# Performance work log

Measured on AMD Instinct MI355X. Metric: run time of the kernel, lower is better.

The kernel has to match this reference:

```python
import math
import jax, jax.numpy as jnp
import numpy as np

H = 8
DIM = 256
HD = DIM // H
SCALE = math.sqrt(HD)
EPS = 1e-16


def _segment_softmax(scores, dst, num_nodes):
    # scores: [E, H], dst: [E] -> softmax over edges sharing the same dst
    m = jax.ops.segment_max(scores, dst, num_segments=num_nodes)  # [N, H]
    m = jnp.where(jnp.isfinite(m), m, 0.0)  # empty segments -> -inf -> 0
    e = jnp.exp(scores - m[dst])
    s = jax.ops.segment_sum(e, dst, num_segments=num_nodes)  # [N, H]
    return e / (s[dst] + EPS)


def _graph_attention(x, edges, wq, bq, wk, bk, wv, bv, wo, bo):
    # x: [N, DIM]; edges: [2, E] (src, dst). Dropout is identity (eval mode).
    N = x.shape[0]
    Q = (x @ wq + bq).reshape(N, H, HD)
    K = (x @ wk + bk).reshape(N, H, HD)
    V = (x @ wv + bv).reshape(N, H, HD)
    src, dst = edges[0], edges[1]
    scores = jnp.einsum('ehd,ehd->eh', Q[dst], K[src]) / SCALE  # [E, H]
    attn = _segment_softmax(scores, dst, N)  # [E, H]
    msgs = V[src] * attn[:, :, None]  # [E, H, HD]
    out = jax.ops.segment_sum(msgs, dst, num_segments=N).reshape(N, DIM)
    return out @ wo + bo


def _linear_params(key, fan_in, fan_out):
    k1, k2 = jax.random.split(key)
    bound = 1.0 / math.sqrt(fan_in)
    w = jax.random.uniform(k1, (fan_in, fan_out), minval=-bound, maxval=bound, dtype=jnp.float32)
    b = jax.random.uniform(k2, (fan_out,), minval=-bound, maxval=bound, dtype=jnp.float32)
    return w, b


def setup_inputs() -> dict:
    key = jax.random.key(0)
    ks = jax.random.split(key, 12)
    n_slot, n_dom = 20000, 1000
    e_slot, e_dom = 320000, 16000
    inp = {
        'slot_x': jax.random.normal(ks[0], (n_slot, DIM), dtype=jnp.float32),
        'domain_x': jax.random.normal(ks[1], (n_dom, DIM), dtype=jnp.float32),
        'slot_edges': jax.random.randint(ks[2], (2, e_slot), 0, n_slot, dtype=jnp.int32),
        'domain_edges': jax.random.randint(ks[3], (2, e_dom), 0, n_dom, dtype=jnp.int32),
    }
    names = ['wq', 'wk', 'wv', 'wo']
    for i, nm in enumerate(names):
        w, b = _linear_params(ks[4 + i], DIM, DIM)
        inp[f'slot_{nm}'] = w
        inp[f'slot_{nm}_b'] = b
    for i, nm in enumerate(names):
        w, b = _linear_params(ks[8 + i], DIM, DIM)
        inp[f'dom_{nm}'] = w
        inp[f'dom_{nm}_b'] = b
    return inp


def reference(slot_x, domain_x, slot_edges, domain_edges,
              slot_wq, slot_wq_b, slot_wk, slot_wk_b, slot_wv, slot_wv_b, slot_wo, slot_wo_b,
              dom_wq, dom_wq_b, dom_wk, dom_wk_b, dom_wv, dom_wv_b, dom_wo, dom_wo_b):
    # slot branch: self-attention on slot graph + identity residual
    slot_out = _graph_attention(slot_x, slot_edges,
                                slot_wq, slot_wq_b, slot_wk, slot_wk_b,
                                slot_wv, slot_wv_b, slot_wo, slot_wo_b) + slot_x
    # domain branch
    dom_out = _graph_attention(domain_x, domain_edges,
                               dom_wq, dom_wq_b, dom_wk, dom_wk_b,
                               dom_wv, dom_wv_b, dom_wo, dom_wo_b) + domain_x
    return slot_out, dom_out
```

## Files before the change

### kernel.cpp

```cpp
#include <hip/hip_runtime.h>
#include <hip/hip_bf16.h>

#define DIM 256
#define INV_SCALE 0.17677669529663687f
#define SM_EPS 1e-16f
#define BM 128
#define BN 64
#define BK 32
#define LDAS 40

typedef unsigned short ushortT;
typedef unsigned int uintT;
typedef __attribute__((ext_vector_type(8))) __bf16 bf16x8;
typedef __attribute__((ext_vector_type(4))) float f32x4;

__device__ __forceinline__ float bf2f(ushortT u) {
    return __uint_as_float(((uintT)u) << 16);
}
__device__ __forceinline__ ushortT f2bf(float f) {
    uintT u = __float_as_uint(f);
    u += 0x7FFFu + ((u >> 16) & 1u);
    return (ushortT)(u >> 16);
}

struct WPack { const void* w[8]; const void* b[8]; };

__device__ __forceinline__ bool sniff_m16(const ushortT* __restrict__ x) {
    int lane = threadIdx.x & 63;
    ushortT u = x[lane * 2];
    int e = (u >> 7) & 0xFF;
    bool sane = ((u & 0x7FFFu) == 0) || (e >= 0x66 && e <= 0x90);
    unsigned long long m = __ballot(sane);
    return __popcll(m) >= 32;
}

__global__ __launch_bounds__(256) void megaA(
        const void* __restrict__ xs, const void* __restrict__ xd,
        const ushortT* __restrict__ sniff_src,
        ushortT* __restrict__ xb_s, ushortT* __restrict__ xb_d,
        WPack pk, ushortT* __restrict__ wT, float* __restrict__ biasF,
        int* __restrict__ cnt_s, int* __restrict__ cnt_d,
        uintT* __restrict__ st_s, uintT* __restrict__ st_d,
        int* __restrict__ done, int* __restrict__ flagWs,
        int n4s, int n4d, int Ns_, int Nd_, int nbN_, int nbD_,
        int nA0, int nA1)
{
    const bool m16 = sniff_m16(sniff_src);
    const int bid = blockIdx.x;
    const int t = threadIdx.x;

    if (bid < nA0 + nA1) {
        const bool d = bid >= nA0;
        const int li = d ? bid - nA0 : bid;
        const int n4 = d ? n4d : n4s;
        const int i = li * 256 + t;
        if (i >= n4) return;
        const void* x = d ? xd : xs;
        ushortT* xb = d ? xb_d : xb_s;
        if (m16) {
            ((ushort4*)xb)[i] = ((const ushort4*)x)[i];
        } else {
            float4 v = ((const float4*)x)[i];
            ushort4 o2;
            o2.x = f2bf(v.x); o2.y = f2bf(v.y); o2.z = f2bf(v.z); o2.w = f2bf(v.w);
            ((ushort4*)xb)[i] = o2;
        }
    } else if (bid < nA0 + nA1 + 128) {
        __shared__ float sh[64][65];
        const int r0 = bid - (nA0 + nA1);
        const int which = r0 >> 4;
        const int tile = r0 & 15;
        const int tr = tile >> 2, tc = tile & 3;
        const void* w = pk.w[which];
        const int tx = t & 63, tg = t >> 6;
        #pragma unroll
        for (int i = 0; i < 16; ++i) {
            const int r = i * 4 + tg;
            const size_t si = (size_t)(tr * 64 + r) * 256 + tc * 64 + tx;
            sh[r][tx] = m16 ? bf2f(((const ushortT*)w)[si]) : ((const float*)w)[si];
        }
        __syncthreads();
        ushortT* o = wT + (size_t)which * 65536;
        #pragma unroll
        for (int i = 0; i < 16; ++i) {
            const int r = i * 4 + tg;
            o[(size_t)(tc * 64 + r) * 256 + tr * 64 + tx] = f2bf(sh[tx][r]);
        }
    } else if (bid < nA0 + nA1 + 136) {
        const int which = bid - (nA0 + nA1 + 128);
        const void* b = pk.b[which];
        float v = m16 ? bf2f(((const ushortT*)b)[t]) : ((const float*)b)[t];
        biasF[which * 256 + t] = v;
    } else {
        const int li = bid - (nA0 + nA1 + 136);
        const int idx = li * 256 + t;
        if (idx < Ns_) { cnt_s[idx] = 0; return; }
        int k = idx - Ns_;
        if (k < Nd_) { cnt_d[k] = 0; return; }
        k -= Nd_;
        if (k < nbN_) { st_s[k] = 0; return; }
        k -= nbN_;
        if (k < nbD_) { st_d[k] = 0; return; }
        k -= nbD_;
        if (k == 0) *done = 0;
        else if (k == 1) *flagWs = m16 ? 1 : 0;
    }
}

__global__ __launch_bounds__(256) void megaB(
        const ushortT* __restrict__ xb_s, const ushortT* __restrict__ xb_d,
        const ushortT* __restrict__ wT, const float* __restrict__ biasF,
        ushortT* __restrict__ qkv_s, ushortT* __restrict__ qkv_d,
        size_t zss, size_t zsd, int Ms, int Md, int nbs_, int nbq_,
        const int* __restrict__ dst_s, const int* __restrict__ dst_d,
        int* __restrict__ cnt_s, int* __restrict__ cnt_d, int Es_, int Ed_)
{
    const int bid = blockIdx.x;
    const int nq = nbq_ * 4;
    if (bid >= nq) {
        const int idx = (bid - nq) * 256 + threadIdx.x;
        if (idx < Es_) atomicAdd(&cnt_s[dst_s[idx]], 1);
        else { int e = idx - Es_; if (e < Ed_) atomicAdd(&cnt_d[dst_d[e]], 1); }
        return;
    }
    const int by  = bid / nbq_;
    const int bx0 = bid % nbq_;
    const bool dom = bx0 >= nbs_;
    const int bx = dom ? bx0 - nbs_ : bx0;
    const ushortT* A = dom ? xb_d : xb_s;
    const int M = dom ? Md : Ms;
    const int wbase = dom ? 4 : 0;
    const size_t zstride = dom ? zsd : zss;
    ushortT* Cb = dom ? qkv_d : qkv_s;

    __shared__ ushortT As[BM * LDAS];
    __shared__ ushortT Bs[3][BN * LDAS];
    const int tid  = threadIdx.x;
    const int wid  = tid >> 6;
    const int lane = tid & 63;
    const int r_i = tid >> 2;
    const int kq8 = (tid & 3) << 3;
    const int m   = lane & 15;
    const int q   = lane >> 4;
    const int row0 = bx * BM;
    const int col0 = by * BN;

    f32x4 acc[3][2][4];
    #pragma unroll
    for (int z = 0; z < 3; ++z)
        #pragma unroll
        for (int i = 0; i < 2; ++i)
            #pragma unroll
            for (int j = 0; j < 4; ++j)
                acc[z][i][j] = (f32x4){0.f, 0.f, 0.f, 0.f};

    const size_t rA0 = (size_t)min(row0 + r_i, M - 1) * DIM;
    const size_t rA1 = (size_t)min(row0 + 64 + r_i, M - 1) * DIM;
    const size_t rB  = (size_t)(col0 + r_i) * DIM;

    for (int k0 = 0; k0 < DIM; k0 += BK) {
        uint4 a0v = *(const uint4*)(A + rA0 + k0 + kq8);
        uint4 a1v = *(const uint4*)(A + rA1 + k0 + kq8);
        uint4 b0v = *(const uint4*)(wT + (size_t)(wbase + 0) * 65536 + rB + k0 + kq8);
        uint4 b1v = *(const uint4*)(wT + (size_t)(wbase + 1) * 65536 + rB + k0 + kq8);
        uint4 b2v = *(const uint4*)(wT + (size_t)(wbase + 2) * 65536 + rB + k0 + kq8);
        __syncthreads();
        *(uint4*)&As[r_i * LDAS + kq8]        = a0v;
        *(uint4*)&As[(64 + r_i) * LDAS + kq8] = a1v;
        *(uint4*)&Bs[0][r_i * LDAS + kq8]     = b0v;
        *(uint4*)&Bs[1][r_i * LDAS + kq8]     = b1v;
        *(uint4*)&Bs[2][r_i * LDAS + kq8]     = b2v;
        __syncthreads();

        bf16x8 af0 = *(const bf16x8*)&As[(wid * 32 + m) * LDAS + q * 8];
        bf16x8 af1 = *(const bf16x8*)&As[(wid * 32 + 16 + m) * LDAS + q * 8];
        #pragma unroll
        for (int j = 0; j < 4; ++j) {
            #pragma unroll
            for (int z = 0; z < 3; ++z) {
                bf16x8 bf = *(const bf16x8*)&Bs[z][(j * 16 + m) * LDAS + q * 8];
                acc[z][0][j] = __builtin_amdgcn_mfma_f32_16x16x32_bf16(af0, bf, acc[z][0][j], 0, 0, 0);
                acc[z][1][j] = __builtin_amdgcn_mfma_f32_16x16x32_bf16(af1, bf, acc[z][1][j], 0, 0, 0);
            }
        }
    }

    #pragma unroll
    for (int z = 0; z < 3; ++z) {
        ushortT* C = Cb + (size_t)z * zstride;
        const float* bias = biasF + (wbase + z) * 256;
        #pragma unroll
        for (int i = 0; i < 2; ++i)
            #pragma unroll
            for (int j = 0; j < 4; ++j) {
                const int col = col0 + j * 16 + m;
                const float bval = bias[col];
                #pragma unroll
                for (int rr = 0; rr < 4; ++rr) {
                    const int row = row0 + wid * 32 + i * 16 + q * 4 + rr;
                    if (row < M)
                        C[(size_t)row * DIM + col] = f2bf(acc[z][i][j][rr] + bval);
                }
            }
    }
}

__device__ __forceinline__ uintT spack(uintT st, uintT v) { return (st << 30) | v; }

__global__ __launch_bounds__(256) void scan_nodes(
        const int* __restrict__ cnt_s, const int* __restrict__ cnt_d,
        uintT* __restrict__ st_s, uintT* __restrict__ st_d,
        int* __restrict__ rp_s, int* __restrict__ rp_d,
        int* __restrict__ cur_s, int* __restrict__ cur_d,
        int Ns_, int Nd_, int nbN_)
{
    __shared__ int sh[256];
    __shared__ int exclS;
    const int b = blockIdx.x;
    const int t = threadIdx.x;
    const bool dom = b >= nbN_;
    const int lb = dom ? b - nbN_ : b;
    const int N = dom ? Nd_ : Ns_;
    const int* cnt = dom ? cnt_d : cnt_s;
    uintT* st = dom ? st_d : st_s;
    int* rp = dom ? rp_d : rp_s;
    int* cur = dom ? cur_d : cur_s;

    const int i = lb * 256 + t;
    const int v = (i < N) ? cnt[i] : 0;
    sh[t] = v;
    __syncthreads();
    for (int off = 1; off < 256; off <<= 1) {
        int u = (t >= off) ? sh[t - off] : 0;
        __syncthreads();
        sh[t] += u;
        __syncthreads();
    }

    if (t == 0) {
        const uintT agg = (uintT)sh[255];
        uintT excl = 0;
        if (lb == 0) {
            __hip_atomic_store(&st[0], spack(2u, agg), __ATOMIC_RELEASE,
                               __HIP_MEMORY_SCOPE_AGENT);
        } else {
            __hip_atomic_store(&st[lb], spack(1u, agg), __ATOMIC_RELEASE,
                               __HIP_MEMORY_SCOPE_AGENT);
            int j = lb - 1;
            while (j >= 0) {
                uintT s = __hip_atomic_load(&st[j], __ATOMIC_ACQUIRE,
                                            __HIP_MEMORY_SCOPE_AGENT);
                uintT tag = s >> 30;
                if (tag == 2u) { excl += s & 0x3FFFFFFFu; break; }
                if (tag == 1u) { excl += s & 0x3FFFFFFFu; --j; }
            }
            __hip_atomic_store(&st[lb], spack(2u, excl + agg), __ATOMIC_RELEASE,
                               __HIP_MEMORY_SCOPE_AGENT);
        }
        exclS = (int)excl;
    }
    __syncthreads();
    const int excl = exclS;
    if (i < N) {
        const int e = excl + ((t == 0) ? 0 : sh[t - 1]);
        rp[i] = e;
        cur[i] = e;
        if (i == N - 1) rp[N] = e + v;
    }
}

__global__ __launch_bounds__(256) void scatter_edges(
        const int* __restrict__ ss, const int* __restrict__ ds,
        const int* __restrict__ sd, const int* __restrict__ dd,
        int* __restrict__ cur_s, int* __restrict__ cur_d,
        int* __restrict__ col_s, int* __restrict__ col_d,
        int Es_, int Ed_)
{
    const int idx = blockIdx.x * 256 + threadIdx.x;
    if (idx < Es_) {
        int pos = atomicAdd(&cur_s[ds[idx]], 1);
        col_s[pos] = ss[idx];
    } else {
        int e = idx - Es_;
        if (e < Ed_) {
            int pos = atomicAdd(&cur_d[dd[e]], 1);
            col_d[pos] = sd[e];
        }
    }
}

__global__ __launch_bounds__(256) void attn_kernel(
        const ushortT* __restrict__ Qs, const ushortT* __restrict__ Ks,
        const ushortT* __restrict__ Vs, const int* __restrict__ rps,
        const int* __restrict__ css, ushortT* __restrict__ aggs,
        const ushortT* __restrict__ Qd_, const ushortT* __restrict__ Kd_,
        const ushortT* __restrict__ Vd_, const int* __restrict__ rpd,
        const int* __restrict__ csd, ushortT* __restrict__ aggd,
        int Ns_, int Ntot)
{
    const int g = blockIdx.x * 4 + (threadIdx.x >> 6);
    if (g >= Ntot) return;
    const bool dom = g >= Ns_;
    const int d = dom ? g - Ns_ : g;
    const int t = threadIdx.x & 63;
    const ushortT* Qb = dom ? Qd_ : Qs;
    const ushortT* Kb = dom ? Kd_ : Ks;
    const ushortT* Vb = dom ? Vd_ : Vs;
    const int* rowptr = dom ? rpd : rps;
    const int* colsrc = dom ? csd : css;
    ushortT* aggb = dom ? aggd : aggs;

    const int t4 = t * 4;
    const size_t cbase = (size_t)d * DIM + t4;
    uint2 qv = *(const uint2*)(Qb + cbase);
    const float q0 = bf2f((ushortT)(qv.x & 0xFFFF)), q1 = bf2f((ushortT)(qv.x >> 16));
    const float q2 = bf2f((ushortT)(qv.y & 0xFFFF)), q3 = bf2f((ushortT)(qv.y >> 16));

    float a0 = 0.f, a1 = 0.f, a2 = 0.f, a3 = 0.f, den = 0.f;

    auto PROC = [&](uint2 kvc, uint2 vvc) {
        float k0 = bf2f((ushortT)(kvc.x & 0xFFFF)), k1 = bf2f((ushortT)(kvc.x >> 16));
        float k2 = bf2f((ushortT)(kvc.y & 0xFFFF)), k3 = bf2f((ushortT)(kvc.y >> 16));
        float p = q0 * k0 + q1 * k1 + q2 * k2 + q3 * k3;
        p += __shfl_xor(p, 1, 8);
        p += __shfl_xor(p, 2, 8);
        p += __shfl_xor(p, 4, 8);
        const float w = __expf(fminf(p * INV_SCALE, 60.0f));
        den += w;
        a0 += w * bf2f((ushortT)(vvc.x & 0xFFFF));
        a1 += w * bf2f((ushortT)(vvc.x >> 16));
        a2 += w * bf2f((ushortT)(vvc.y & 0xFFFF));
        a3 += w * bf2f((ushortT)(vvc.y >> 16));
    };

    const int beg = rowptr[d], end = rowptr[d + 1];
    int i = beg;
    for (; i + 4 <= end; i += 4) {
        const int s0 = colsrc[i], s1 = colsrc[i + 1];
        const int s2 = colsrc[i + 2], s3 = colsrc[i + 3];
        const size_t b0 = (size_t)s0 * DIM + t4, b1 = (size_t)s1 * DIM + t4;
        const size_t b2 = (size_t)s2 * DIM + t4, b3 = (size_t)s3 * DIM + t4;
        uint2 k0v = *(const uint2*)(Kb + b0), v0v = *(const uint2*)(Vb + b0);
        uint2 k1v = *(const uint2*)(Kb + b1), v1v = *(const uint2*)(Vb + b1);
        uint2 k2v = *(const uint2*)(Kb + b2), v2v = *(const uint2*)(Vb + b2);
        uint2 k3v = *(const uint2*)(Kb + b3), v3v = *(const uint2*)(Vb + b3);
        PROC(k0v, v0v); PROC(k1v, v1v); PROC(k2v, v2v); PROC(k3v, v3v);
    }
    for (; i < end; ++i) {
        const size_t sb = (size_t)colsrc[i] * DIM + t4;
        uint2 kv = *(const uint2*)(Kb + sb);
        uint2 vv = *(const uint2*)(Vb + sb);
        PROC(kv, vv);
    }

    const float r = 1.0f / (den + SM_EPS);
    ushort4 o;
    o.x = f2bf(a0 * r); o.y = f2bf(a1 * r); o.z = f2bf(a2 * r); o.w = f2bf(a3 * r);
    *(ushort4*)(aggb + cbase) = o;
}

__global__ __launch_bounds__(256) void gemm_out(
        const ushortT* __restrict__ As_, const ushortT* __restrict__ Ad_,
        const ushortT* __restrict__ wT, const float* __restrict__ biasF,
        const void* __restrict__ xs, const void* __restrict__ xd,
        void* __restrict__ dout, int Ms, int Md, int nbs,
        const int* __restrict__ flag)
{
    const bool dom = (int)blockIdx.x >= nbs;
    const int bx = dom ? blockIdx.x - nbs : blockIdx.x;
    const ushortT* A = dom ? Ad_ : As_;
    const int M = dom ? Md : Ms;
    const int widx = 3 + (dom ? 4 : 0);
    const ushortT* BT = wT + (size_t)widx * 65536;
    const float* bias = biasF + widx * 256;
    const void* res = dom ? xd : xs;
    const size_t outOff = dom ? (size_t)Ms * DIM : 0;

    __shared__ ushortT As2[BM * LDAS];
    __shared__ ushortT Bs2[BN * LDAS];
    const int tid  = threadIdx.x;
    const int wid  = tid >> 6;
    const int lane = tid & 63;
    const int r_i = tid >> 2;
    const int kq8 = (tid & 3) << 3;
    const int m   = lane & 15;
    const int q   = lane >> 4;
    const int row0 = bx * BM;
    const int col0 = blockIdx.y * BN;

    f32x4 acc[2][4];
    #pragma unroll
    for (int i = 0; i < 2; ++i)
        #pragma unroll
        for (int j = 0; j < 4; ++j) acc[i][j] = (f32x4){0.f, 0.f, 0.f, 0.f};

    const size_t rA0 = (size_t)min(row0 + r_i, M - 1) * DIM;
    const size_t rA1 = (size_t)min(row0 + 64 + r_i, M - 1) * DIM;
    const size_t rB  = (size_t)(col0 + r_i) * DIM;

    for (int k0 = 0; k0 < DIM; k0 += BK) {
        uint4 a0v = *(const uint4*)(A + rA0 + k0 + kq8);
        uint4 a1v = *(const uint4*)(A + rA1 + k0 + kq8);
        uint4 bv  = *(const uint4*)(BT + rB + k0 + kq8);
        __syncthreads();
        *(uint4*)&As2[r_i * LDAS + kq8]        = a0v;
        *(uint4*)&As2[(64 + r_i) * LDAS + kq8] = a1v;
        *(uint4*)&Bs2[r_i * LDAS + kq8]        = bv;
        __syncthreads();

        bf16x8 af0 = *(const bf16x8*)&As2[(wid * 32 + m) * LDAS + q * 8];
        bf16x8 af1 = *(const bf16x8*)&As2[(wid * 32 + 16 + m) * LDAS + q * 8];
        #pragma unroll
        for (int j = 0; j < 4; ++j) {
            bf16x8 bf = *(const bf16x8*)&Bs2[(j * 16 + m) * LDAS + q * 8];
            acc[0][j] = __builtin_amdgcn_mfma_f32_16x16x32_bf16(af0, bf, acc[0][j], 0, 0, 0);
            acc[1][j] = __builtin_amdgcn_mfma_f32_16x16x32_bf16(af1, bf, acc[1][j], 0, 0, 0);
        }
    }

    const bool m16 = (*flag != 0);
    #pragma unroll
    for (int i = 0; i < 2; ++i)
        #pragma unroll
        for (int j = 0; j < 4; ++j) {
            const int col = col0 + j * 16 + m;
            const float bval = bias[col];
            #pragma unroll
            for (int r = 0; r < 4; ++r) {
                const int row = row0 + wid * 32 + i * 16 + q * 4 + r;
                if (row < M) {
                    const size_t ridx = (size_t)row * DIM + col;
                    float v = acc[i][j][r] + bval;
                    v += m16 ? bf2f(((const ushortT*)res)[ridx])
                             : ((const float*)res)[ridx];
                    if (m16) ((ushortT*)dout)[outOff + ridx] = f2bf(v);
                    else     ((float*)dout)[outOff + ridx] = v;
                }
            }
        }
}

extern "C" void kernel_launch(void* const* d_in, const int* in_sizes, int n_in,
                              void* d_out, int out_size, void* d_ws, size_t ws_size,
                              hipStream_t stream)
{
    const void* slot_x = d_in[0];
    const void* dom_x  = d_in[1];
    const int* slot_edges = (const int*)d_in[2];
    const int* dom_edges  = (const int*)d_in[3];
    const int Ns = in_sizes[0] / DIM;
    const int Nd = in_sizes[1] / DIM;
    const int Es = in_sizes[2] / 2;
    const int Ed = in_sizes[3] / 2;

    WPack pk;
    for (int i = 0; i < 8; ++i) { pk.w[i] = d_in[4 + 2 * i]; pk.b[i] = d_in[5 + 2 * i]; }

    char* p = (char*)d_ws;
    size_t o = 0;
    auto take = [&](size_t b) { void* r = p + o; o = (o + b + 255) & ~(size_t)255; return r; };
    const size_t ndS = (size_t)Ns * DIM;
    const size_t ndD = (size_t)Nd * DIM;
    ushortT* xb_s  = (ushortT*)take(ndS * 2);
    ushortT* qkv_s = (ushortT*)take(3 * ndS * 2);
    ushortT* agg_s = (ushortT*)take(ndS * 2);
    ushortT* xb_d  = (ushortT*)take(ndD * 2);
    ushortT* qkv_d = (ushortT*)take(3 * ndD * 2);
    ushortT* agg_d = (ushortT*)take(ndD * 2);
    ushortT* wT    = (ushortT*)take(8 * 65536 * 2);
    float*   biasF = (float*)take(8 * 256 * 4);
    int* rp_s  = (int*)take((size_t)(Ns + 1) * 4);
    int* cur_s = (int*)take((size_t)Ns * 4);
    int* cnt_s = (int*)take((size_t)Ns * 4);
    int* col_s = (int*)take((size_t)Es * 4);
    int* rp_d  = (int*)take((size_t)(Nd + 1) * 4);
    int* cur_d = (int*)take((size_t)Nd * 4);
    int* cnt_d = (int*)take((size_t)Nd * 4);
    int* col_d = (int*)take((size_t)Ed * 4);
    uintT* st_s = (uintT*)take(512 * 4);
    uintT* st_d = (uintT*)take(256 * 4);
    int* done   = (int*)take(256);
    int* flagWs = (int*)take(256);

    const int* src_s = slot_edges;
    const int* dst_s = slot_edges + Es;
    const int* src_d = dom_edges;
    const int* dst_d = dom_edges + Ed;

    const int n4s = Ns * DIM / 4, n4d = Nd * DIM / 4;
    const int nbN = (Ns + 255) / 256;
    const int nbD = (Nd + 255) / 256;
    const int nbs = (Ns + BM - 1) / BM;
    const int nbd = (Nd + BM - 1) / BM;
    const int nbq = nbs + nbd;

    const int nA0 = (n4s + 255) / 256;
    const int nA1 = (n4d + 255) / 256;
    const int nZ  = (Ns + Nd + nbN + nbD + 2 + 255) / 256;
    hipLaunchKernelGGL(megaA, dim3(nA0 + nA1 + 136 + nZ), dim3(256), 0, stream,
                       slot_x, dom_x, (const ushortT*)slot_x, xb_s, xb_d,
                       pk, wT, biasF, cnt_s, cnt_d, st_s, st_d, done, flagWs,
                       n4s, n4d, Ns, Nd, nbN, nbD, nA0, nA1);

    const int nCnt = (Es + Ed + 255) / 256;
    hipLaunchKernelGGL(megaB, dim3(nbq * 4 + nCnt), dim3(256), 0, stream,
                       xb_s, xb_d, wT, biasF, qkv_s, qkv_d, ndS, ndD,
                       Ns, Nd, nbs, nbq, dst_s, dst_d, cnt_s, cnt_d, Es, Ed);

    hipLaunchKernelGGL(scan_nodes, dim3(nbN + nbD), dim3(256), 0, stream,
                       cnt_s, cnt_d, st_s, st_d, rp_s, rp_d, cur_s, cur_d,
                       Ns, Nd, nbN);
    hipLaunchKernelGGL(scatter_edges, dim3(nCnt), dim3(256), 0, stream,
                       src_s, dst_s, src_d, dst_d, cur_s, cur_d, col_s, col_d,
                       Es, Ed);

    const int Ntot = Ns + Nd;
    hipLaunchKernelGGL(attn_kernel, dim3((Ntot + 3) / 4), dim3(256), 0, stream,
                       qkv_s, qkv_s + ndS, qkv_s + 2 * ndS, rp_s, col_s, agg_s,
                       qkv_d, qkv_d + ndD, qkv_d + 2 * ndD, rp_d, col_d, agg_d,
                       Ns, Ntot);

    hipLaunchKernelGGL(gemm_out, dim3(nbq, DIM / BN), dim3(256), 0, stream,
                       agg_s, agg_d, wT, biasF, slot_x, dom_x, d_out,
                       Ns, Nd, nbs, flagWs);
}
```

Measured before the change: 262.3 us.

## Drop LDS staging in QKV and output GEMMs, load MFMA fragments directly from global

Both the fused QKV projection and the output projection GEMMs stop staging tiles through shared memory. Each wave now loads its bf16 A and B fragments straight from global memory into registers and feeds the MFMAs, which removes the per-k-step __syncthreads barriers and LDS traffic. Tiles shrink from 128 rows to 64, so the grids have twice as many blocks. In exchange, A rows are re-read from global/L2 by each of the four waves in a block instead of being shared, and the fragment loads are strided rather than coalesced.

New measurement: 283.7 us. +8.2%, slower.

```diff
diff --git a/kernel.cpp b/kernel.cpp
--- a/kernel.cpp
+++ b/kernel.cpp
@@ -4,10 +4,6 @@
 #define DIM 256
 #define INV_SCALE 0.17677669529663687f
 #define SM_EPS 1e-16f
-#define BM 128
-#define BN 64
-#define BK 32
-#define LDAS 40
 
 typedef unsigned short ushortT;
 typedef unsigned int uintT;
@@ -133,75 +129,57 @@
     const size_t zstride = dom ? zsd : zss;
     ushortT* Cb = dom ? qkv_d : qkv_s;
 
-    __shared__ ushortT As[BM * LDAS];
-    __shared__ ushortT Bs[3][BN * LDAS];
     const int tid  = threadIdx.x;
     const int wid  = tid >> 6;
     const int lane = tid & 63;
-    const int r_i = tid >> 2;
-    const int kq8 = (tid & 3) << 3;
-    const int m   = lane & 15;
-    const int q   = lane >> 4;
-    const int row0 = bx * BM;
-    const int col0 = by * BN;
-
-    f32x4 acc[3][2][4];
+    const int m    = lane & 15;
+    const int q    = lane >> 4;
+    const int row0 = bx * 64;
+    const int colw = by * 64 + wid * 16 + m;
+
+    f32x4 acc[3][4];
     #pragma unroll
     for (int z = 0; z < 3; ++z)
         #pragma unroll
-        for (int i = 0; i < 2; ++i)
+        for (int i = 0; i < 4; ++i)
+            acc[z][i] = (f32x4){0.f, 0.f, 0.f, 0.f};
+
+    size_t ra[4];
+    #pragma unroll
+    for (int i = 0; i < 4; ++i)
+        ra[i] = (size_t)min(row0 + i * 16 + m, M - 1) * DIM + q * 8;
+
+    const ushortT* Bp = wT + (size_t)wbase * 65536 + (size_t)colw * DIM + q * 8;
+
+    for (int k0 = 0; k0 < DIM; k0 += 32) {
+        bf16x8 af[4];
+        #pragma unroll
+        for (int i = 0; i < 4; ++i)
+            af[i] = *(const bf16x8*)(A + ra[i] + k0);
+        bf16x8 bf[3];
+        #pragma unroll
+        for (int z = 0; z < 3; ++z)
+            bf[z] = *(const bf16x8*)(Bp + (size_t)z * 65536 + k0);
+        #pragma unroll
+        for (int z = 0; z < 3; ++z)
             #pragma unroll
-            for (int j = 0; j < 4; ++j)
-                acc[z][i][j] = (f32x4){0.f, 0.f, 0.f, 0.f};
-
-    const size_t rA0 = (size_t)min(row0 + r_i, M - 1) * DIM;
-    const size_t rA1 = (size_t)min(row0 + 64 + r_i, M - 1) * DIM;
-    const size_t rB  = (size_t)(col0 + r_i) * DIM;
-
-    for (int k0 = 0; k0 < DIM; k0 += BK) {
-        uint4 a0v = *(const uint4*)(A + rA0 + k0 + kq8);
-        uint4 a1v = *(const uint4*)(A + rA1 + k0 + kq8);
-        uint4 b0v = *(const uint4*)(wT + (size_t)(wbase + 0) * 65536 + rB + k0 + kq8);
-        uint4 b1v = *(const uint4*)(wT + (size_t)(wbase + 1) * 65536 + rB + k0 + kq8);
-        uint4 b2v = *(const uint4*)(wT + (size_t)(wbase + 2) * 65536 + rB + k0 + kq8);
-        __syncthreads();
-        *(uint4*)&As[r_i * LDAS + kq8]        = a0v;
-        *(uint4*)&As[(64 + r_i) * LDAS + kq8] = a1v;
-        *(uint4*)&Bs[0][r_i * LDAS + kq8]     = b0v;
-        *(uint4*)&Bs[1][r_i * LDAS + kq8]     = b1v;
-        *(uint4*)&Bs[2][r_i * LDAS + kq8]     = b2v;
-        __syncthreads();
-
-        bf16x8 af0 = *(const bf16x8*)&As[(wid * 32 + m) * LDAS + q * 8];
-        bf16x8 af1 = *(const bf16x8*)&As[(wid * 32 + 16 + m) * LDAS + q * 8];
-        #pragma unroll
-        for (int j = 0; j < 4; ++j) {
-            #pragma unroll
-            for (int z = 0; z < 3; ++z) {
-                bf16x8 bf = *(const bf16x8*)&Bs[z][(j * 16 + m) * LDAS + q * 8];
-                acc[z][0][j] = __builtin_amdgcn_mfma_f32_16x16x32_bf16(af0, bf, acc[z][0][j], 0, 0, 0);
-                acc[z][1][j] = __builtin_amdgcn_mfma_f32_16x16x32_bf16(af1, bf, acc[z][1][j], 0, 0, 0);
-            }
-        }
+            for (int i = 0; i < 4; ++i)
+                acc[z][i] = __builtin_amdgcn_mfma_f32_16x16x32_bf16(af[i], bf[z], acc[z][i], 0, 0, 0);
     }
 
     #pragma unroll
     for (int z = 0; z < 3; ++z) {
         ushortT* C = Cb + (size_t)z * zstride;
-        const float* bias = biasF + (wbase + z) * 256;
-        #pragma unroll
-        for (int i = 0; i < 2; ++i)
+        const float bval = biasF[(wbase + z) * 256 + colw];
+        #pragma unroll
+        for (int i = 0; i < 4; ++i) {
             #pragma unroll
-            for (int j = 0; j < 4; ++j) {
-                const int col = col0 + j * 16 + m;
-                const float bval = bias[col];
-                #pragma unroll
-                for (int rr = 0; rr < 4; ++rr) {
-                    const int row = row0 + wid * 32 + i * 16 + q * 4 + rr;
-                    if (row < M)
-                        C[(size_t)row * DIM + col] = f2bf(acc[z][i][j][rr] + bval);
-                }
+            for (int rr = 0; rr < 4; ++rr) {
+                const int row = row0 + i * 16 + q * 4 + rr;
+                if (row < M)
+                    C[(size_t)row * DIM + colw] = f2bf(acc[z][i][rr] + bval);
             }
+        }
     }
 }
 
@@ -376,68 +354,53 @@
     const void* res = dom ? xd : xs;
     const size_t outOff = dom ? (size_t)Ms * DIM : 0;
 
-    __shared__ ushortT As2[BM * LDAS];
-    __shared__ ushortT Bs2[BN * LDAS];
     const int tid  = threadIdx.x;
     const int wid  = tid >> 6;
     const int lane = tid & 63;
-    const int r_i = tid >> 2;
-    const int kq8 = (tid & 3) << 3;
-    const int m   = lane & 15;
-    const int q   = lane >> 4;
-    const int row0 = bx * BM;
-    const int col0 = blockIdx.y * BN;
-
-    f32x4 acc[2][4];
-    #pragma unroll
-    for (int i = 0; i < 2; ++i)
-        #pragma unroll
-        for (int j = 0; j < 4; ++j) acc[i][j] = (f32x4){0.f, 0.f, 0.f, 0.f};
-
-    const size_t rA0 = (size_t)min(row0 + r_i, M - 1) * DIM;
-    const size_t rA1 = (size_t)min(row0 + 64 + r_i, M - 1) * DIM;
-    const size_t rB  = (size_t)(col0 + r_i) * DIM;
-
-    for (int k0 = 0; k0 < DIM; k0 += BK) {
-        uint4 a0v = *(const uint4*)(A + rA0 + k0 + kq8);
-        uint4 a1v = *(const uint4*)(A + rA1 + k0 + kq8);
-        uint4 bv  = *(const uint4*)(BT + rB + k0 + kq8);
-        __syncthreads();
-        *(uint4*)&As2[r_i * LDAS + kq8]        = a0v;
-        *(uint4*)&As2[(64 + r_i) * LDAS + kq8] = a1v;
-        *(uint4*)&Bs2[r_i * LDAS + kq8]        = bv;
-        __syncthreads();
-
-        bf16x8 af0 = *(const bf16x8*)&As2[(wid * 32 + m) * LDAS + q * 8];
-        bf16x8 af1 = *(const bf16x8*)&As2[(wid * 32 + 16 + m) * LDAS + q * 8];
-        #pragma unroll
-        for (int j = 0; j < 4; ++j) {
-            bf16x8 bf = *(const bf16x8*)&Bs2[(j * 16 + m) * LDAS + q * 8];
-            acc[0][j] = __builtin_amdgcn_mfma_f32_16x16x32_bf16(af0, bf, acc[0][j], 0, 0, 0);
-            acc[1][j] = __builtin_amdgcn_mfma_f32_16x16x32_bf16(af1, bf, acc[1][j], 0, 0, 0);
-        }
+    const int m    = lane & 15;
+    const int q    = lane >> 4;
+    const int row0 = bx * 64;
+    const int colw = blockIdx.y * 64 + wid * 16 + m;
+
+    f32x4 acc[4];
+    #pragma unroll
+    for (int i = 0; i < 4; ++i) acc[i] = (f32x4){0.f, 0.f, 0.f, 0.f};
+
+    size_t ra[4];
+    #pragma unroll
+    for (int i = 0; i < 4; ++i)
+        ra[i] = (size_t)min(row0 + i * 16 + m, M - 1) * DIM + q * 8;
+
+    const ushortT* Bp = BT + (size_t)colw * DIM + q * 8;
+
+    for (int k0 = 0; k0 < DIM; k0 += 32) {
+        bf16x8 af[4];
+        #pragma unroll
+        for (int i = 0; i < 4; ++i)
+            af[i] = *(const bf16x8*)(A + ra[i] + k0);
+        bf16x8 bf = *(const bf16x8*)(Bp + k0);
+        #pragma unroll
+        for (int i = 0; i < 4; ++i)
+            acc[i] = __builtin_amdgcn_mfma_f32_16x16x32_bf16(af[i], bf, acc[i], 0, 0, 0);
     }
 
     const bool m16 = (*flag != 0);
-    #pragma unroll
-    for (int i = 0; i < 2; ++i)
-        #pragma unroll
-        for (int j = 0; j < 4; ++j) {
-            const int col = col0 + j * 16 + m;
-            const float bval = bias[col];
-            #pragma unroll
-            for (int r = 0; r < 4; ++r) {
-                const int row = row0 + wid * 32 + i * 16 + q * 4 + r;
-                if (row < M) {
-                    const size_t ridx = (size_t)row * DIM + col;
-                    float v = acc[i][j][r] + bval;
-                    v += m16 ? bf2f(((const ushortT*)res)[ridx])
-                             : ((const float*)res)[ridx];
-                    if (m16) ((ushortT*)dout)[outOff + ridx] = f2bf(v);
-                    else     ((float*)dout)[outOff + ridx] = v;
-                }
+    const float bval = bias[colw];
+    #pragma unroll
+    for (int i = 0; i < 4; ++i) {
+        #pragma unroll
+        for (int r = 0; r < 4; ++r) {
+            const int row = row0 + i * 16 + q * 4 + r;
+            if (row < M) {
+                const size_t ridx = (size_t)row * DIM + colw;
+                float v = acc[i][r] + bval;
+                v += m16 ? bf2f(((const ushortT*)res)[ridx])
+                         : ((const float*)res)[ridx];
+                if (m16) ((ushortT*)dout)[outOff + ridx] = f2bf(v);
+                else     ((float*)dout)[outOff + ridx] = v;
             }
         }
+    }
 }
 
 extern "C" void kernel_launch(void* const* d_in, const int* in_sizes, int n_in,
@@ -490,8 +453,8 @@
     const int n4s = Ns * DIM / 4, n4d = Nd * DIM / 4;
     const int nbN = (Ns + 255) / 256;
     const int nbD = (Nd + 255) / 256;
-    const int nbs = (Ns + BM - 1) / BM;
-    const int nbd = (Nd + BM - 1) / BM;
+    const int nbs = (Ns + 63) / 64;
+    const int nbd = (Nd + 63) / 64;
     const int nbq = nbs + nbd;
 
     const int nA0 = (n4s + 255) / 256;
@@ -520,7 +483,7 @@
                        qkv_d, qkv_d + ndD, qkv_d + 2 * ndD, rp_d, col_d, agg_d,
                        Ns, Ntot);
 
-    hipLaunchKernelGGL(gemm_out, dim3(nbq, DIM / BN), dim3(256), 0, stream,
+    hipLaunchKernelGGL(gemm_out, dim3(nbq, DIM / 64), dim3(256), 0, stream,
                        agg_s, agg_d, wT, biasF, slot_x, dom_x, d_out,
                        Ns, Nd, nbs, flagWs);
 }
```
